# Kernel optimization log

Hardware: AMD Instinct MI355X
Metric: run time of the kernel (lower is better)

The kernel has to match this reference:

```python
import jax, jax.numpy as jnp
import numpy as np

DIM = 1024
NUM_HEADS = 16
HEAD_DIM = DIM // NUM_HEADS
ROPE_BASE = 10000.0


def _rope_cos_sin(seq_len, head_dim, dtype):
    inv_freq = 1.0 / (ROPE_BASE ** (jnp.arange(0, head_dim, 2, dtype=jnp.float32) / head_dim))
    t = jnp.arange(seq_len, dtype=jnp.float32)
    freqs = jnp.einsum('i,j->ij', t, inv_freq)          # (S, head_dim/2)
    emb = jnp.concatenate([freqs, freqs], axis=-1)       # (S, head_dim)
    return jnp.cos(emb).astype(dtype), jnp.sin(emb).astype(dtype)


def _rotate_half(x):
    x1, x2 = jnp.split(x, 2, axis=-1)
    return jnp.concatenate([-x2, x1], axis=-1)


def setup_inputs() -> dict:
    key = jax.random.key(0)
    k1, k2, k3 = jax.random.split(key, 3)
    B, S = 2, 2048
    x = jax.random.normal(k1, (B, S, DIM), dtype=jnp.float32)
    w_qkv = jax.random.normal(k2, (3 * DIM, DIM), dtype=jnp.float32) * (DIM ** -0.5)
    w_out = jax.random.normal(k3, (DIM, DIM), dtype=jnp.float32) * (DIM ** -0.5)
    return {"x": x, "w_qkv": w_qkv, "w_out": w_out}


def reference(x, w_qkv, w_out):
    B, S, _ = x.shape
    scale = HEAD_DIM ** -0.5

    qkv = jnp.einsum('bsd,ed->bse', x, w_qkv)                 # (B, S, 3*DIM)
    qkv = qkv.reshape(B, S, 3, NUM_HEADS, HEAD_DIM)
    qkv = jnp.transpose(qkv, (2, 0, 3, 1, 4))                  # (3, B, H, S, hd)
    Q, K, V = qkv[0], qkv[1], qkv[2]

    cos, sin = _rope_cos_sin(S, HEAD_DIM, x.dtype)             # (S, hd)
    Q = Q * cos + _rotate_half(Q) * sin
    K = K * cos + _rotate_half(K) * sin

    scores = jnp.einsum('bhqd,bhkd->bhqk', Q, K) * scale       # (B, H, S, S)
    causal = jnp.tril(jnp.ones((S, S), dtype=bool))
    scores = jnp.where(causal[None, None], scores, jnp.asarray(-1e9, scores.dtype))
    attn = jax.nn.softmax(scores, axis=-1)

    out = jnp.einsum('bhqk,bhkd->bhqd', attn, V)               # (B, H, S, hd)
    out = jnp.transpose(out, (0, 2, 1, 3)).reshape(B, S, DIM)
    out = jnp.einsum('bsd,ed->bse', out, w_out)
    return out
```

## Files before the change

### kernel.cpp

```cpp
#include <hip/hip_runtime.h>
#include <hip/hip_bf16.h>

#define DIM 1024
#define NHEADS 16
#define HD 64
#define BB 2
#define SS 2048
#define MTOT (BB*SS)
#define SCALE 0.125f
#define QSCALE 0.1803368801111204f

typedef __attribute__((ext_vector_type(8))) short bf16x8;
typedef __attribute__((ext_vector_type(4))) float f32x4;

__device__ __forceinline__ float bf2f(short u) {
  union { float f; unsigned int i; } v;
  v.i = ((unsigned int)(unsigned short)u) << 16;
  return v.f;
}
__device__ __forceinline__ short f2bf(float f) {
  union { float f; unsigned int i; } v; v.f = f;
  unsigned int r = v.i + 0x7fffu + ((v.i >> 16) & 1u);
  return (short)(r >> 16);
}
__device__ __forceinline__ unsigned int cvtpk_bf16(float lo, float hi) {
  unsigned int r;
  asm("v_cvt_pk_bf16_f32 %0, %1, %2" : "=v"(r) : "v"(lo), "v"(hi));
  return r;
}

__global__ void cvt_kernel(const float* __restrict__ in, short* __restrict__ out, int n) {
  int nq = n >> 2;
  int stride = gridDim.x * blockDim.x;
  for (int q = blockIdx.x * blockDim.x + threadIdx.x; q < nq; q += stride) {
    float4 v = *(const float4*)(in + (size_t)q * 4);
    short4 o;
    o.x = f2bf(v.x); o.y = f2bf(v.y); o.z = f2bf(v.z); o.w = f2bf(v.w);
    *(short4*)(out + (size_t)q * 4) = o;
  }
}

__global__ void rope_table_kernel(float* __restrict__ ct, float* __restrict__ st) {
  int i = blockIdx.x * blockDim.x + threadIdx.x;
  if (i >= SS * 32) return;
  int s = i >> 5, j = i & 31;
  float inv = 1.0f / powf(10000.0f, (float)(2 * j) / 64.0f);
  float ang = (float)s * inv;
  ct[i] = cosf(ang);
  st[i] = sinf(ang);
}

template<bool OUT_F32>
__global__ __launch_bounds__(256) void gemm_bt(
    const short* __restrict__ A, const short* __restrict__ B,
    void* __restrict__ C, int M, int N, int K) {
  __shared__ short As[128][40];
  __shared__ short Bs[128][40];
  const int tid = threadIdx.x;
  const int lane = tid & 63;
  const int wid = tid >> 6;
  const int wm = (wid >> 1) * 64, wn = (wid & 1) * 64;
  const int m0 = blockIdx.y * 128, n0 = blockIdx.x * 128;
  const int row = lane & 15, kg = (lane >> 4) * 8;

  f32x4 acc[4][4];
#pragma unroll
  for (int m = 0; m < 4; m++)
#pragma unroll
    for (int n = 0; n < 4; n++) acc[m][n] = (f32x4){0.f, 0.f, 0.f, 0.f};

  const int r0 = tid >> 2;
  const int c0 = (tid & 3) * 8;
  for (int kk = 0; kk < K; kk += 32) {
    __syncthreads();
    bf16x8 a0 = *(const bf16x8*)(A + (size_t)(m0 + r0) * K + kk + c0);
    bf16x8 a1 = *(const bf16x8*)(A + (size_t)(m0 + 64 + r0) * K + kk + c0);
    bf16x8 b0 = *(const bf16x8*)(B + (size_t)(n0 + r0) * K + kk + c0);
    bf16x8 b1 = *(const bf16x8*)(B + (size_t)(n0 + 64 + r0) * K + kk + c0);
    *(bf16x8*)(&As[r0][c0]) = a0;
    *(bf16x8*)(&As[64 + r0][c0]) = a1;
    *(bf16x8*)(&Bs[r0][c0]) = b0;
    *(bf16x8*)(&Bs[64 + r0][c0]) = b1;
    __syncthreads();
    bf16x8 af[4], bfr[4];
#pragma unroll
    for (int m = 0; m < 4; m++) af[m] = *(const bf16x8*)(&As[wm + m * 16 + row][kg]);
#pragma unroll
    for (int n = 0; n < 4; n++) bfr[n] = *(const bf16x8*)(&Bs[wn + n * 16 + row][kg]);
#pragma unroll
    for (int m = 0; m < 4; m++)
#pragma unroll
      for (int n = 0; n < 4; n++)
        acc[m][n] = __builtin_amdgcn_mfma_f32_16x16x32_bf16(af[m], bfr[n], acc[m][n], 0, 0, 0);
  }
  const int orow = (lane >> 4) * 4, ocol = lane & 15;
#pragma unroll
  for (int m = 0; m < 4; m++)
#pragma unroll
    for (int n = 0; n < 4; n++)
#pragma unroll
      for (int r = 0; r < 4; r++) {
        int gr = m0 + wm + m * 16 + orow + r;
        int gc = n0 + wn + n * 16 + ocol;
        if (OUT_F32) ((float*)C)[(size_t)gr * N + gc] = acc[m][n][r];
        else         ((short*)C)[(size_t)gr * N + gc] = f2bf(acc[m][n][r]);
      }
}

__global__ __launch_bounds__(256) void rope_kernel(
    const short* __restrict__ qkv, const float* __restrict__ ct, const float* __restrict__ st,
    short* __restrict__ Q, short* __restrict__ K) {
  int bh = blockIdx.y;
  int b = bh >> 4, h = bh & 15;
  int s0 = blockIdx.x * 64;
  int t = threadIdx.x;
  int rl = t >> 2;
  int d8 = (t & 3) * 8;
  int s = s0 + rl;
  size_t inbase = ((size_t)(b * SS + s)) * 3072 + h * 64 + d8;
  size_t outbase = ((size_t)bh * SS + s) * 64 + d8;
  float c[8], sn[8];
#pragma unroll
  for (int j = 0; j < 8; j++) { c[j] = ct[s * 32 + d8 + j]; sn[j] = st[s * 32 + d8 + j]; }
  {
    bf16x8 x1 = *(const bf16x8*)(qkv + inbase);
    bf16x8 x2 = *(const bf16x8*)(qkv + inbase + 32);
    bf16x8 o1, o2;
#pragma unroll
    for (int j = 0; j < 8; j++) {
      float a = bf2f(x1[j]), bb = bf2f(x2[j]);
      o1[j] = f2bf((a * c[j] - bb * sn[j]) * QSCALE);
      o2[j] = f2bf((bb * c[j] + a * sn[j]) * QSCALE);
    }
    *(bf16x8*)(Q + outbase) = o1;
    *(bf16x8*)(Q + outbase + 32) = o2;
  }
  {
    bf16x8 x1 = *(const bf16x8*)(qkv + inbase + 1024);
    bf16x8 x2 = *(const bf16x8*)(qkv + inbase + 1024 + 32);
    bf16x8 o1, o2;
#pragma unroll
    for (int j = 0; j < 8; j++) {
      float a = bf2f(x1[j]), bb = bf2f(x2[j]);
      o1[j] = f2bf(a * c[j] - bb * sn[j]);
      o2[j] = f2bf(bb * c[j] + a * sn[j]);
    }
    *(bf16x8*)(K + outbase) = o1;
    *(bf16x8*)(K + outbase + 32) = o2;
  }
}

__global__ __launch_bounds__(256) void vtrans_kernel(const short* __restrict__ qkv, short* __restrict__ Vt) {
  __shared__ short ls[64][72];
  int bh = blockIdx.y, b = bh >> 4, h = bh & 15;
  int s0 = blockIdx.x * 64;
  int t = threadIdx.x;
#pragma unroll
  for (int p = 0; p < 2; p++) {
    int idx = p * 256 + t;
    int r = idx >> 3, c8 = (idx & 7) * 8;
    *(bf16x8*)(&ls[r][c8]) =
        *(const bf16x8*)(qkv + ((size_t)(b * SS + s0 + r)) * 3072 + 2048 + h * 64 + c8);
  }
  __syncthreads();
  int dl = t >> 2, sg = (t & 3) * 16;
  int c = sg >> 5, hi = (sg >> 4) & 1;
  short tmp[16];
#pragma unroll
  for (int j = 0; j < 16; j++) tmp[j] = ls[sg + j][dl];
  size_t rowbase = ((size_t)bh * 64 + dl) * SS + s0;
#pragma unroll
  for (int g = 0; g < 4; g++) {
    short4 o = { tmp[4 * g], tmp[4 * g + 1], tmp[4 * g + 2], tmp[4 * g + 3] };
    *(short4*)(Vt + rowbase + c * 32 + g * 8 + hi * 4) = o;
  }
}

__global__ __launch_bounds__(256) void attn_kernel(
    const short* __restrict__ Qp, const short* __restrict__ Kp, const short* __restrict__ Vt,
    short* __restrict__ O) {
  __shared__ short Ks[64][72];
  __shared__ short Vs[64][72];
  int flat = blockIdx.x;
  int wk = (flat & 7) * 128 + (flat >> 3);
  int bh = wk >> 5;
  int qt = 31 - (wk & 31);
  int b = bh >> 4, h = bh & 15;
  int q0 = qt * 64;
  int tid = threadIdx.x, lane = tid & 63, w = tid >> 6;
  int row = lane & 15, grp = lane >> 4;
  int q = q0 + w * 16 + row;

  bf16x8 qf0, qf1;
  {
    size_t qb = ((size_t)bh * SS + q) * 64 + grp * 8;
    qf0 = *(const bf16x8*)(Qp + qb);
    qf1 = *(const bf16x8*)(Qp + qb + 32);
  }
  f32x4 acc[4];
#pragma unroll
  for (int d = 0; d < 4; d++) acc[d] = (f32x4){0.f, 0.f, 0.f, 0.f};
  float m = -1e30f, l = 0.f;

  const int ksr = tid >> 3;
  const int ksc = (tid & 7) * 8;
  const short* Kbase = Kp + (size_t)bh * SS * 64;
  const short* Vbase = Vt + (size_t)bh * 64 * SS;

  for (int kt = 0; kt <= qt; kt++) {
    int kv0 = kt * 64;
    __syncthreads();
#pragma unroll
    for (int p2 = 0; p2 < 2; p2++) {
      int r = p2 * 32 + ksr;
      *(bf16x8*)(&Ks[r][ksc]) = *(const bf16x8*)(Kbase + (size_t)(kv0 + r) * 64 + ksc);
      *(bf16x8*)(&Vs[r][ksc]) = *(const bf16x8*)(Vbase + (size_t)r * SS + kv0 + ksc);
    }
    __syncthreads();
    bool last = (kt == qt);
    float sv[4][4];
#pragma unroll
    for (int n = 0; n < 4; n++) {
      if (last && n > w) {
#pragma unroll
        for (int r = 0; r < 4; r++) sv[n][r] = -1e30f;
        continue;
      }
      f32x4 sf = (f32x4){0.f, 0.f, 0.f, 0.f};
      bf16x8 kf0 = *(const bf16x8*)(&Ks[n * 16 + row][grp * 8]);
      bf16x8 kf1 = *(const bf16x8*)(&Ks[n * 16 + row][grp * 8 + 32]);
      sf = __builtin_amdgcn_mfma_f32_16x16x32_bf16(kf0, qf0, sf, 0, 0, 0);
      sf = __builtin_amdgcn_mfma_f32_16x16x32_bf16(kf1, qf1, sf, 0, 0, 0);
#pragma unroll
      for (int r = 0; r < 4; r++) sv[n][r] = sf[r];
    }
    if (last) {
#pragma unroll
      for (int n = 0; n < 4; n++)
#pragma unroll
        for (int r = 0; r < 4; r++) {
          int kv = kv0 + n * 16 + grp * 4 + r;
          if (kv > q) sv[n][r] = -1e30f;
        }
    }
    float pmax = -1e30f;
#pragma unroll
    for (int n = 0; n < 4; n++)
#pragma unroll
      for (int r = 0; r < 4; r++) pmax = fmaxf(pmax, sv[n][r]);
    pmax = fmaxf(pmax, __shfl_xor(pmax, 16));
    pmax = fmaxf(pmax, __shfl_xor(pmax, 32));
    float mnew = fmaxf(m, pmax);
    float resc = __builtin_amdgcn_exp2f(m - mnew);
    m = mnew;
    float p[4][4];
    float psum = 0.f;
#pragma unroll
    for (int n = 0; n < 4; n++)
#pragma unroll
      for (int r = 0; r < 4; r++) {
        p[n][r] = __builtin_amdgcn_exp2f(sv[n][r] - m);
        psum += p[n][r];
      }
    psum += __shfl_xor(psum, 16);
    psum += __shfl_xor(psum, 32);
    l = l * resc + psum;
#pragma unroll
    for (int d = 0; d < 4; d++)
#pragma unroll
      for (int r = 0; r < 4; r++) acc[d][r] *= resc;
#pragma unroll
    for (int c = 0; c < 2; c++) {
      union { unsigned int u[4]; bf16x8 v; } pu;
      pu.u[0] = cvtpk_bf16(p[2 * c][0], p[2 * c][1]);
      pu.u[1] = cvtpk_bf16(p[2 * c][2], p[2 * c][3]);
      pu.u[2] = cvtpk_bf16(p[2 * c + 1][0], p[2 * c + 1][1]);
      pu.u[3] = cvtpk_bf16(p[2 * c + 1][2], p[2 * c + 1][3]);
#pragma unroll
      for (int dm = 0; dm < 4; dm++) {
        bf16x8 vf = *(const bf16x8*)(&Vs[dm * 16 + row][c * 32 + grp * 8]);
        acc[dm] = __builtin_amdgcn_mfma_f32_16x16x32_bf16(vf, pu.v, acc[dm], 0, 0, 0);
      }
    }
  }
  float linv = 1.0f / l;
  size_t ob = ((size_t)(b * SS + q)) * 1024 + h * 64 + grp * 4;
#pragma unroll
  for (int dm = 0; dm < 4; dm++) {
    union { unsigned int u[2]; short4 s; } ou;
    ou.u[0] = cvtpk_bf16(acc[dm][0] * linv, acc[dm][1] * linv);
    ou.u[1] = cvtpk_bf16(acc[dm][2] * linv, acc[dm][3] * linv);
    *(short4*)(O + ob + dm * 16) = ou.s;
  }
}

extern "C" void kernel_launch(void* const* d_in, const int* in_sizes, int n_in,
                              void* d_out, int out_size, void* d_ws, size_t ws_size,
                              hipStream_t stream) {
  (void)in_sizes; (void)n_in; (void)out_size; (void)ws_size;
  const float* x     = (const float*)d_in[0];
  const float* w_qkv = (const float*)d_in[1];
  const float* w_out = (const float*)d_in[2];
  float* out = (float*)d_out;

  char* ws = (char*)d_ws;
  size_t off = 0;
  auto alloc = [&](size_t bytes) -> void* {
    void* p = ws + off;
    off += (bytes + 255) & ~(size_t)255;
    return p;
  };
  short* xb    = (short*)alloc((size_t)MTOT * DIM * 2);
  short* wqkvb = (short*)alloc((size_t)3072 * 1024 * 2);
  short* woutb = (short*)alloc((size_t)1024 * 1024 * 2);
  short* qkvb  = (short*)alloc((size_t)MTOT * 3072 * 2);
  short* Qb    = (short*)alloc((size_t)32 * SS * 64 * 2);
  short* Kb    = (short*)alloc((size_t)32 * SS * 64 * 2);
  short* Vtb   = (short*)alloc((size_t)32 * 64 * SS * 2);
  float* ct    = (float*)alloc((size_t)SS * 32 * 4);
  float* st    = (float*)alloc((size_t)SS * 32 * 4);
  short* attnb = xb;

  cvt_kernel<<<2048, 256, 0, stream>>>(x, xb, MTOT * DIM);
  cvt_kernel<<<2048, 256, 0, stream>>>(w_qkv, wqkvb, 3072 * 1024);
  cvt_kernel<<<1024, 256, 0, stream>>>(w_out, woutb, 1024 * 1024);
  rope_table_kernel<<<SS * 32 / 256, 256, 0, stream>>>(ct, st);
  gemm_bt<false><<<dim3(3072 / 128, MTOT / 128), 256, 0, stream>>>(xb, wqkvb, qkvb, MTOT, 3072, 1024);
  rope_kernel<<<dim3(SS / 64, 32), 256, 0, stream>>>(qkvb, ct, st, Qb, Kb);
  vtrans_kernel<<<dim3(SS / 64, 32), 256, 0, stream>>>(qkvb, Vtb);
  attn_kernel<<<1024, 256, 0, stream>>>(Qb, Kb, Vtb, attnb);
  gemm_bt<true><<<dim3(1024 / 128, MTOT / 128), 256, 0, stream>>>(attnb, woutb, out, MTOT, 1024, 1024);
}
```

Measured before the change: 157.2 us.

## Use direct global-to-LDS loads in GEMM and halve attention query tile

The GEMM staging now issues global_load_lds instructions that copy tiles straight into shared memory, skipping the register round trip, and drops the padded LDS rows to fit that instruction's layout. The attention kernel moves from 64-query tiles with 4 waves to 32-query tiles with 2 waves, doubling the grid and adjusting the causal diagonal masking, for finer load balance and more resident blocks. Risks: the unpadded LDS layout may cause bank conflicts on MFMA fragment reads, and smaller attention tiles reload each K/V tile for half as many queries.

```diff
diff --git a/kernel.cpp b/kernel.cpp
--- a/kernel.cpp
+++ b/kernel.cpp
@@ -28,6 +28,11 @@
   asm("v_cvt_pk_bf16_f32 %0, %1, %2" : "=v"(r) : "v"(lo), "v"(hi));
   return r;
 }
+__device__ __forceinline__ void async_load16(const short* g, short* l) {
+  __builtin_amdgcn_global_load_lds(
+      (const __attribute__((address_space(1))) unsigned int*)g,
+      (__attribute__((address_space(3))) unsigned int*)l, 16, 0, 0);
+}
 
 __global__ void cvt_kernel(const float* __restrict__ in, short* __restrict__ out, int n) {
   int nq = n >> 2;
@@ -54,14 +59,16 @@
 __global__ __launch_bounds__(256) void gemm_bt(
     const short* __restrict__ A, const short* __restrict__ B,
     void* __restrict__ C, int M, int N, int K) {
-  __shared__ short As[128][40];
-  __shared__ short Bs[128][40];
+  __shared__ __align__(16) short As[128][32];
+  __shared__ __align__(16) short Bs[128][32];
   const int tid = threadIdx.x;
   const int lane = tid & 63;
   const int wid = tid >> 6;
   const int wm = (wid >> 1) * 64, wn = (wid & 1) * 64;
   const int m0 = blockIdx.y * 128, n0 = blockIdx.x * 128;
   const int row = lane & 15, kg = (lane >> 4) * 8;
+  const int lrow = lane >> 2;
+  const int lcol = (lane & 3) * 8;
 
   f32x4 acc[4][4];
 #pragma unroll
@@ -69,18 +76,14 @@
 #pragma unroll
     for (int n = 0; n < 4; n++) acc[m][n] = (f32x4){0.f, 0.f, 0.f, 0.f};
 
-  const int r0 = tid >> 2;
-  const int c0 = (tid & 3) * 8;
   for (int kk = 0; kk < K; kk += 32) {
     __syncthreads();
-    bf16x8 a0 = *(const bf16x8*)(A + (size_t)(m0 + r0) * K + kk + c0);
-    bf16x8 a1 = *(const bf16x8*)(A + (size_t)(m0 + 64 + r0) * K + kk + c0);
-    bf16x8 b0 = *(const bf16x8*)(B + (size_t)(n0 + r0) * K + kk + c0);
-    bf16x8 b1 = *(const bf16x8*)(B + (size_t)(n0 + 64 + r0) * K + kk + c0);
-    *(bf16x8*)(&As[r0][c0]) = a0;
-    *(bf16x8*)(&As[64 + r0][c0]) = a1;
-    *(bf16x8*)(&Bs[r0][c0]) = b0;
-    *(bf16x8*)(&Bs[64 + r0][c0]) = b1;
+#pragma unroll
+    for (int i = 0; i < 2; i++) {
+      int base = i * 64 + wid * 16;
+      async_load16(A + (size_t)(m0 + base + lrow) * K + kk + lcol, &As[base][0]);
+      async_load16(B + (size_t)(n0 + base + lrow) * K + kk + lcol, &Bs[base][0]);
+    }
     __syncthreads();
     bf16x8 af[4], bfr[4];
 #pragma unroll
@@ -176,17 +179,17 @@
   }
 }
 
-__global__ __launch_bounds__(256) void attn_kernel(
+__global__ __launch_bounds__(128) void attn_kernel(
     const short* __restrict__ Qp, const short* __restrict__ Kp, const short* __restrict__ Vt,
     short* __restrict__ O) {
   __shared__ short Ks[64][72];
   __shared__ short Vs[64][72];
   int flat = blockIdx.x;
-  int wk = (flat & 7) * 128 + (flat >> 3);
-  int bh = wk >> 5;
-  int qt = 31 - (wk & 31);
+  int wk = (flat & 7) * 256 + (flat >> 3);
+  int bh = wk >> 6;
+  int qi = 63 - (wk & 63);
   int b = bh >> 4, h = bh & 15;
-  int q0 = qt * 64;
+  int q0 = qi * 32;
   int tid = threadIdx.x, lane = tid & 63, w = tid >> 6;
   int row = lane & 15, grp = lane >> 4;
   int q = q0 + w * 16 + row;
@@ -207,21 +210,24 @@
   const short* Kbase = Kp + (size_t)bh * SS * 64;
   const short* Vbase = Vt + (size_t)bh * 64 * SS;
 
-  for (int kt = 0; kt <= qt; kt++) {
+  const int ktlast = qi >> 1;
+  const int d16 = (qi & 1) * 2;
+
+  for (int kt = 0; kt <= ktlast; kt++) {
     int kv0 = kt * 64;
     __syncthreads();
 #pragma unroll
-    for (int p2 = 0; p2 < 2; p2++) {
-      int r = p2 * 32 + ksr;
+    for (int p2 = 0; p2 < 4; p2++) {
+      int r = p2 * 16 + ksr;
       *(bf16x8*)(&Ks[r][ksc]) = *(const bf16x8*)(Kbase + (size_t)(kv0 + r) * 64 + ksc);
       *(bf16x8*)(&Vs[r][ksc]) = *(const bf16x8*)(Vbase + (size_t)r * SS + kv0 + ksc);
     }
     __syncthreads();
-    bool last = (kt == qt);
+    bool last = (kt == ktlast);
     float sv[4][4];
 #pragma unroll
     for (int n = 0; n < 4; n++) {
-      if (last && n > w) {
+      if (last && n > d16 + w) {
 #pragma unroll
         for (int r = 0; r < 4; r++) sv[n][r] = -1e30f;
         continue;
@@ -328,6 +334,6 @@
   gemm_bt<false><<<dim3(3072 / 128, MTOT / 128), 256, 0, stream>>>(xb, wqkvb, qkvb, MTOT, 3072, 1024);
   rope_kernel<<<dim3(SS / 64, 32), 256, 0, stream>>>(qkvb, ct, st, Qb, Kb);
   vtrans_kernel<<<dim3(SS / 64, 32), 256, 0, stream>>>(qkvb, Vtb);
-  attn_kernel<<<1024, 256, 0, stream>>>(Qb, Kb, Vtb, attnb);
+  attn_kernel<<<2048, 128, 0, stream>>>(Qb, Kb, Vtb, attnb);
   gemm_bt<true><<<dim3(1024 / 128, MTOT / 128), 256, 0, stream>>>(attnb, woutb, out, MTOT, 1024, 1024);
 }
```

After: 164.0 us. 4.3% more time.
